# Kernel optimization log

Hardware: AMD Instinct MI355X
Metric: run time of the kernel (lower is better)

The kernel has to match this reference:

```python
import jax, jax.numpy as jnp
import numpy as np

HEAD_DIM = 32
KERNEL = 3
DILATION = 2
SCALE = HEAD_DIM ** -0.5


def _unfold(x, kernel, dilation):
    # x: [B, C, H, W] -> patches [B, C, kernel*kernel, H, W]
    # matches nn.Unfold(kernel, dilation, padding=dilation*(kernel-1)//2, stride=1)
    B, C, H, W = x.shape
    pad = dilation * (kernel - 1) // 2
    xp = jnp.pad(x, ((0, 0), (0, 0), (pad, pad), (pad, pad)))
    patches = jnp.stack(
        [xp[:, :, i * dilation:i * dilation + H, j * dilation:j * dilation + W]
         for i in range(kernel) for j in range(kernel)],
        axis=2,
    )
    return patches  # [B, C, k*k, H, W]


def setup_inputs() -> dict:
    key = jax.random.key(0)
    kq, kk, kv = jax.random.split(key, 3)
    shape = (8, 192, 56, 56)
    return {
        "q": jax.random.normal(kq, shape, dtype=jnp.float32),
        "k": jax.random.normal(kk, shape, dtype=jnp.float32),
        "v": jax.random.normal(kv, shape, dtype=jnp.float32),
    }


def reference(q, k, v):
    B, d, H, W = q.shape
    h = d // HEAD_DIM
    kk2 = KERNEL * KERNEL
    HW = H * W

    # q: [B, h, hd, HW]
    qh = q.reshape(B, h, HEAD_DIM, HW)
    # unfolded k/v: [B, h, hd, k*k, HW]
    kp = _unfold(k, KERNEL, DILATION).reshape(B, h, HEAD_DIM, kk2, HW)
    vp = _unfold(v, KERNEL, DILATION).reshape(B, h, HEAD_DIM, kk2, HW)

    attn = jnp.einsum('bhdn,bhdkn->bhnk', qh, kp) * SCALE
    attn = jax.nn.softmax(attn, axis=-1)
    # dropout p=0 (eval): no-op

    # [B, h, HW, hd]
    out = jnp.einsum('bhnk,bhdkn->bhnd', attn, vp)
    # transpose(1,2).reshape(B,H,W,d): channel order = head-major
    out = out.transpose(0, 2, 1, 3).reshape(B, H, W, d)
    return out
```

## Files before the change

kernel.cpp:

```cpp
#include <hip/hip_runtime.h>

#define NH 6
#define HEAD_DIM 32
#define CCH 192
#define HH 56
#define WW 56
#define HWSZ (HH * WW)
#define KPOS 9
#define SCALE 0.17677669529663687f
#define XPAD 61
#define ROWSZ (HEAD_DIM * XPAD)

__global__ __launch_bounds__(256, 3) void dilate_attn_lds(
    const float* __restrict__ q,
    const float* __restrict__ k,
    const float* __restrict__ v,
    float* __restrict__ out)
{
    __shared__ float ks[3 * ROWSZ];
    __shared__ float vs[3 * ROWSZ];

    const int bh = blockIdx.x % 48;
    const int y  = blockIdx.x / 48;
    const int t  = threadIdx.x;

    const int px = t >> 2;
    const int c  = t & 3;
    const bool active = px < WW;

    float qreg[8];
    if (active) {
        const float* qb = q + ((size_t)bh * HEAD_DIM + 8 * c) * HWSZ + y * WW + px;
#pragma unroll
        for (int j = 0; j < 8; j++) qreg[j] = qb[j * HWSZ];
    }

    const size_t plane = (size_t)bh * HEAD_DIM * HWSZ;
#pragma unroll
    for (int r = 0; r < 3; r++) {
        const int sy = y + 2 * r - 2;
        float* kd = ks + r * ROWSZ;
        float* vd = vs + r * ROWSZ;
        if (sy >= 0 && sy < HH) {
            const float* kg = k + plane + sy * WW;
            const float* vg = v + plane + sy * WW;
#pragma unroll
            for (int i = 0; i < 7; i++) {
                const int idx = t + 256 * i;
                const int d = idx / WW;
                const int x = idx - d * WW;
                const float kvv = kg[d * HWSZ + x];
                const float vvv = vg[d * HWSZ + x];
                kd[d * XPAD + x + 2] = kvv;
                vd[d * XPAD + x + 2] = vvv;
            }
            if (t < 128) {
                const int d  = t >> 2;
                const int xc = t & 3;
                const int xp = (xc < 2) ? xc : (56 + xc);
                kd[d * XPAD + xp] = 0.0f;
                vd[d * XPAD + xp] = 0.0f;
            }
        } else {
#pragma unroll
            for (int i = 0; i < 8; i++) {
                const int idx = t + 256 * i;
                if (idx < ROWSZ) { kd[idx] = 0.0f; vd[idx] = 0.0f; }
            }
        }
    }
    __syncthreads();

    if (!active) return;

    float lg[KPOS];
#pragma unroll
    for (int r = 0; r < 3; r++) {
        const float* kr = ks + r * ROWSZ + (8 * c) * XPAD + px;
        float a0 = 0.f, a1 = 0.f, a2 = 0.f;
#pragma unroll
        for (int j = 0; j < 8; j++) {
            const float* p = kr + j * XPAD;
            const float qj = qreg[j];
            a0 = fmaf(qj, p[0], a0);
            a1 = fmaf(qj, p[2], a1);
            a2 = fmaf(qj, p[4], a2);
        }
        lg[3 * r + 0] = a0;
        lg[3 * r + 1] = a1;
        lg[3 * r + 2] = a2;
    }

#pragma unroll
    for (int kk = 0; kk < KPOS; kk++) {
        float s = lg[kk];
        s += __shfl_xor(s, 1);
        s += __shfl_xor(s, 2);
        lg[kk] = s * SCALE;
    }

    float m = lg[0];
#pragma unroll
    for (int kk = 1; kk < KPOS; kk++) m = fmaxf(m, lg[kk]);
    float ssum = 0.f;
    float w[KPOS];
#pragma unroll
    for (int kk = 0; kk < KPOS; kk++) {
        w[kk] = __expf(lg[kk] - m);
        ssum += w[kk];
    }
    const float inv = 1.f / ssum;
#pragma unroll
    for (int kk = 0; kk < KPOS; kk++) w[kk] *= inv;

    float acc[8];
#pragma unroll
    for (int j = 0; j < 8; j++) acc[j] = 0.f;
#pragma unroll
    for (int r = 0; r < 3; r++) {
        const float* vr = vs + r * ROWSZ + (8 * c) * XPAD + px;
        const float w0 = w[3 * r + 0];
        const float w1 = w[3 * r + 1];
        const float w2 = w[3 * r + 2];
#pragma unroll
        for (int j = 0; j < 8; j++) {
            const float* p = vr + j * XPAD;
            float a = acc[j];
            a = fmaf(w0, p[0], a);
            a = fmaf(w1, p[2], a);
            a = fmaf(w2, p[4], a);
            acc[j] = a;
        }
    }

    const int h = bh % NH;
    const int b = bh / NH;
    float* ob = out + ((size_t)((b * HH + y) * WW + px)) * CCH
                    + h * HEAD_DIM + 8 * c;
    reinterpret_cast<float4*>(ob)[0] = make_float4(acc[0], acc[1], acc[2], acc[3]);
    reinterpret_cast<float4*>(ob)[1] = make_float4(acc[4], acc[5], acc[6], acc[7]);
}

extern "C" void kernel_launch(void* const* d_in, const int* in_sizes, int n_in,
                              void* d_out, int out_size, void* d_ws, size_t ws_size,
                              hipStream_t stream) {
    const float* q = (const float*)d_in[0];
    const float* k = (const float*)d_in[1];
    const float* v = (const float*)d_in[2];
    float* out = (float*)d_out;

    const int blocks = 48 * HH;
    dilate_attn_lds<<<blocks, 256, 0, stream>>>(q, k, v, out);
}
```

Measured before the change: 108.2 us.

## Process two same-parity output rows per block to share staged K/V rows

Each block now handles two output rows y0 and y0+2 with 512 threads, staging four dilated K/V source rows in LDS instead of three per single row. This cuts redundant global loads of K/V (two of the three rows are shared) and halves the block count. It raises LDS use per block to about 62KB, which may limit occupancy, and out-of-range rows are zero-filled via predicated loads.

```diff
diff --git a/kernel.cpp b/kernel.cpp
--- a/kernel.cpp
+++ b/kernel.cpp
@@ -10,85 +10,84 @@
 #define SCALE 0.17677669529663687f
 #define XPAD 61
 #define ROWSZ (HEAD_DIM * XPAD)
+#define NROWS 4
+#define PAIRS 14
 
-__global__ __launch_bounds__(256, 3) void dilate_attn_lds(
+__global__ __launch_bounds__(512, 4) void dilate_attn_pair(
     const float* __restrict__ q,
     const float* __restrict__ k,
     const float* __restrict__ v,
     float* __restrict__ out)
 {
-    __shared__ float ks[3 * ROWSZ];
-    __shared__ float vs[3 * ROWSZ];
+    __shared__ float ks[NROWS * ROWSZ];
+    __shared__ float vs[NROWS * ROWSZ];
 
-    const int bh = blockIdx.x % 48;
-    const int y  = blockIdx.x / 48;
-    const int t  = threadIdx.x;
+    const int bh       = blockIdx.x % 48;
+    const int pair_lin = blockIdx.x / 48;
+    const int parity   = pair_lin / PAIRS;
+    const int p        = pair_lin % PAIRS;
+    const int y0       = 4 * p + parity;
+    const int t        = threadIdx.x;
 
-    const int px = t >> 2;
-    const int c  = t & 3;
-    const bool active = px < WW;
+    const size_t plane = (size_t)bh * HEAD_DIM * HWSZ;
+#pragma unroll
+    for (int i = 0; i < 14; i++) {
+        const int e   = t + 512 * i;
+        const int r   = e / 1792;
+        const int rem = e - r * 1792;
+        const int d   = rem / WW;
+        const int x   = rem - d * WW;
+        const int sy  = y0 - 2 + 2 * r;
+        const bool okr = (sy >= 0) & (sy < HH);
+        const size_t g = plane + (size_t)d * HWSZ + (okr ? sy : 0) * WW + x;
+        const float kvv = okr ? k[g] : 0.0f;
+        const float vvv = okr ? v[g] : 0.0f;
+        const int a = r * ROWSZ + d * XPAD + x + 2;
+        ks[a] = kvv;
+        vs[a] = vvv;
+    }
+    {
+        const int r  = t >> 7;
+        const int rs = t & 127;
+        const int d  = rs >> 2;
+        const int xc = rs & 3;
+        const int xp = (xc < 2) ? xc : (56 + xc);
+        ks[r * ROWSZ + d * XPAD + xp] = 0.0f;
+        vs[r * ROWSZ + d * XPAD + xp] = 0.0f;
+    }
+    __syncthreads();
+
+    const int w2 = t >> 8;
+    const int tt = t & 255;
+    const int px = tt >> 2;
+    const int c  = tt & 3;
+    if (px >= WW) return;
+
+    const int y = y0 + 2 * w2;
 
     float qreg[8];
-    if (active) {
-        const float* qb = q + ((size_t)bh * HEAD_DIM + 8 * c) * HWSZ + y * WW + px;
+    {
+        const float* qb = q + plane + (size_t)(8 * c) * HWSZ + y * WW + px;
 #pragma unroll
         for (int j = 0; j < 8; j++) qreg[j] = qb[j * HWSZ];
     }
 
-    const size_t plane = (size_t)bh * HEAD_DIM * HWSZ;
-#pragma unroll
-    for (int r = 0; r < 3; r++) {
-        const int sy = y + 2 * r - 2;
-        float* kd = ks + r * ROWSZ;
-        float* vd = vs + r * ROWSZ;
-        if (sy >= 0 && sy < HH) {
-            const float* kg = k + plane + sy * WW;
-            const float* vg = v + plane + sy * WW;
-#pragma unroll
-            for (int i = 0; i < 7; i++) {
-                const int idx = t + 256 * i;
-                const int d = idx / WW;
-                const int x = idx - d * WW;
-                const float kvv = kg[d * HWSZ + x];
-                const float vvv = vg[d * HWSZ + x];
-                kd[d * XPAD + x + 2] = kvv;
-                vd[d * XPAD + x + 2] = vvv;
-            }
-            if (t < 128) {
-                const int d  = t >> 2;
-                const int xc = t & 3;
-                const int xp = (xc < 2) ? xc : (56 + xc);
-                kd[d * XPAD + xp] = 0.0f;
-                vd[d * XPAD + xp] = 0.0f;
-            }
-        } else {
-#pragma unroll
-            for (int i = 0; i < 8; i++) {
-                const int idx = t + 256 * i;
-                if (idx < ROWSZ) { kd[idx] = 0.0f; vd[idx] = 0.0f; }
-            }
-        }
-    }
-    __syncthreads();
-
-    if (!active) return;
-
     float lg[KPOS];
 #pragma unroll
-    for (int r = 0; r < 3; r++) {
-        const float* kr = ks + r * ROWSZ + (8 * c) * XPAD + px;
+    for (int rr = 0; rr < 3; rr++) {
+        const float* kr = ks + (w2 + rr) * ROWSZ + (8 * c) * XPAD + px;
         float a0 = 0.f, a1 = 0.f, a2 = 0.f;
 #pragma unroll
         for (int j = 0; j < 8; j++) {
-            const float* p = kr + j * XPAD;
+            const float* pp = kr + j * XPAD;
             const float qj = qreg[j];
-            a0 = fmaf(qj, p[0], a0);
-            a1 = fmaf(qj, p[2], a1);
-            a2 = fmaf(qj, p[4], a2);
+            a0 = fmaf(qj, pp[0], a0);
+            a1 = fmaf(qj, pp[2], a1);
+            a2 = fmaf(qj, pp[4], a2);
         }
-        lg[3 * r + 0] = a0;
-        lg[3 * r + 1] = a1;
-        lg[3 * r + 2] = a2;
+        lg[3 * rr + 0] = a0;
+        lg[3 * rr + 1] = a1;
+        lg[3 * rr + 2] = a2;
     }
 
 #pragma unroll
@@ -117,18 +116,18 @@
 #pragma unroll
     for (int j = 0; j < 8; j++) acc[j] = 0.f;
 #pragma unroll
-    for (int r = 0; r < 3; r++) {
-        const float* vr = vs + r * ROWSZ + (8 * c) * XPAD + px;
-        const float w0 = w[3 * r + 0];
-        const float w1 = w[3 * r + 1];
-        const float w2 = w[3 * r + 2];
+    for (int rr = 0; rr < 3; rr++) {
+        const float* vr = vs + (w2 + rr) * ROWSZ + (8 * c) * XPAD + px;
+        const float w0 = w[3 * rr + 0];
+        const float w1 = w[3 * rr + 1];
+        const float w2f = w[3 * rr + 2];
 #pragma unroll
         for (int j = 0; j < 8; j++) {
-            const float* p = vr + j * XPAD;
+            const float* pp = vr + j * XPAD;
             float a = acc[j];
-            a = fmaf(w0, p[0], a);
-            a = fmaf(w1, p[2], a);
-            a = fmaf(w2, p[4], a);
+            a = fmaf(w0,  pp[0], a);
+            a = fmaf(w1,  pp[2], a);
+            a = fmaf(w2f, pp[4], a);
             acc[j] = a;
         }
     }
@@ -149,6 +148,6 @@
     const float* v = (const float*)d_in[2];
     float* out = (float*)d_out;
 
-    const int blocks = 48 * HH;
-    dilate_attn_lds<<<blocks, 256, 0, stream>>>(q, k, v, out);
+    const int blocks = 48 * 2 * PAIRS;
+    dilate_attn_pair<<<blocks, 512, 0, stream>>>(q, k, v, out);
 }
```

New measurement: 116.5 us. 7.7% more time.

## Process four same-parity rows per block with rolling LDS K/V ring buffer

Applied to the files above, without the earlier changes.

Each block now handles four output rows of the same parity (stride 2), keeping a three-slot ring of K/V rows in LDS. Only one new K/V row is loaded per output row instead of three, and the next row's loads are prefetched into registers while the current row computes. This cuts redundant global reads of K and V by about a factor of three. In exchange the grid shrinks to 672 blocks, each with extra barriers and more register pressure under a tighter launch bound.

```diff
diff --git a/kernel.cpp b/kernel.cpp
--- a/kernel.cpp
+++ b/kernel.cpp
@@ -10,135 +10,175 @@
 #define SCALE 0.17677669529663687f
 #define XPAD 61
 #define ROWSZ (HEAD_DIM * XPAD)
+#define JROWS 4
+#define STRIPS 7
 
-__global__ __launch_bounds__(256, 3) void dilate_attn_lds(
+__global__ __launch_bounds__(256, 4) void dilate_attn_roll(
     const float* __restrict__ q,
     const float* __restrict__ k,
     const float* __restrict__ v,
     float* __restrict__ out)
 {
-    __shared__ float ks[3 * ROWSZ];
-    __shared__ float vs[3 * ROWSZ];
+    __shared__ float ks[3][ROWSZ];
+    __shared__ float vs[3][ROWSZ];
 
-    const int bh = blockIdx.x % 48;
-    const int y  = blockIdx.x / 48;
-    const int t  = threadIdx.x;
+    const int bh     = blockIdx.x % 48;
+    const int ps     = blockIdx.x / 48;
+    const int parity = ps / STRIPS;
+    const int s      = ps % STRIPS;
+    const int y0     = parity + 8 * s;
+    const int t      = threadIdx.x;
 
+    const size_t plane = (size_t)bh * HEAD_DIM * HWSZ;
     const int px = t >> 2;
     const int c  = t & 3;
     const bool active = px < WW;
 
-    float qreg[8];
-    if (active) {
-        const float* qb = q + ((size_t)bh * HEAD_DIM + 8 * c) * HWSZ + y * WW + px;
+    int sd[7], sx[7];
 #pragma unroll
-        for (int j = 0; j < 8; j++) qreg[j] = qb[j * HWSZ];
+    for (int i = 0; i < 7; i++) {
+        const int e = t + 256 * i;
+        sd[i] = e / WW;
+        sx[i] = e - sd[i] * WW;
     }
 
-    const size_t plane = (size_t)bh * HEAD_DIM * HWSZ;
+    float qcur[8];
+    if (active) {
+        const float* qb = q + plane + (size_t)(8 * c) * HWSZ + (size_t)y0 * WW + px;
+#pragma unroll
+        for (int j = 0; j < 8; j++) qcur[j] = qb[j * HWSZ];
+    }
+
+    for (int e = t; e < 3 * HEAD_DIM * 4; e += 256) {
+        const int slot = e >> 7;
+        const int rr   = e & 127;
+        const int d    = rr >> 2;
+        const int xc   = rr & 3;
+        const int xp   = (xc < 2) ? xc : (56 + xc);
+        ks[slot][d * XPAD + xp] = 0.0f;
+        vs[slot][d * XPAD + xp] = 0.0f;
+    }
+
+    float kpre[7], vpre[7];
 #pragma unroll
     for (int r = 0; r < 3; r++) {
-        const int sy = y + 2 * r - 2;
-        float* kd = ks + r * ROWSZ;
-        float* vd = vs + r * ROWSZ;
-        if (sy >= 0 && sy < HH) {
-            const float* kg = k + plane + sy * WW;
-            const float* vg = v + plane + sy * WW;
+        const int ky   = y0 - 2 + 2 * r;
+        const bool okr = (ky >= 0) && (ky < HH);
 #pragma unroll
-            for (int i = 0; i < 7; i++) {
-                const int idx = t + 256 * i;
-                const int d = idx / WW;
-                const int x = idx - d * WW;
-                const float kvv = kg[d * HWSZ + x];
-                const float vvv = vg[d * HWSZ + x];
-                kd[d * XPAD + x + 2] = kvv;
-                vd[d * XPAD + x + 2] = vvv;
-            }
-            if (t < 128) {
-                const int d  = t >> 2;
-                const int xc = t & 3;
-                const int xp = (xc < 2) ? xc : (56 + xc);
-                kd[d * XPAD + xp] = 0.0f;
-                vd[d * XPAD + xp] = 0.0f;
-            }
-        } else {
+        for (int i = 0; i < 7; i++) {
+            const size_t g = plane + (size_t)sd[i] * HWSZ + (size_t)(okr ? ky : 0) * WW + sx[i];
+            kpre[i] = okr ? k[g] : 0.0f;
+            vpre[i] = okr ? v[g] : 0.0f;
+        }
 #pragma unroll
-            for (int i = 0; i < 8; i++) {
-                const int idx = t + 256 * i;
-                if (idx < ROWSZ) { kd[idx] = 0.0f; vd[idx] = 0.0f; }
-            }
+        for (int i = 0; i < 7; i++) {
+            const int a = sd[i] * XPAD + sx[i] + 2;
+            ks[r][a] = kpre[i];
+            vs[r][a] = vpre[i];
         }
     }
     __syncthreads();
 
-    if (!active) return;
+    float qnxt[8];
+#pragma unroll
+    for (int j = 0; j < JROWS; j++) {
+        const int y = y0 + 2 * j;
 
-    float lg[KPOS];
+        if (j < 3) {
+            const int ky   = y0 + 4 + 2 * j;
+            const bool okr = (ky < HH);
 #pragma unroll
-    for (int r = 0; r < 3; r++) {
-        const float* kr = ks + r * ROWSZ + (8 * c) * XPAD + px;
-        float a0 = 0.f, a1 = 0.f, a2 = 0.f;
+            for (int i = 0; i < 7; i++) {
+                const size_t g = plane + (size_t)sd[i] * HWSZ + (size_t)(okr ? ky : 0) * WW + sx[i];
+                kpre[i] = okr ? k[g] : 0.0f;
+                vpre[i] = okr ? v[g] : 0.0f;
+            }
+            if (active) {
+                const float* qb = q + plane + (size_t)(8 * c) * HWSZ + (size_t)(y + 2) * WW + px;
 #pragma unroll
-        for (int j = 0; j < 8; j++) {
-            const float* p = kr + j * XPAD;
-            const float qj = qreg[j];
-            a0 = fmaf(qj, p[0], a0);
-            a1 = fmaf(qj, p[2], a1);
-            a2 = fmaf(qj, p[4], a2);
+                for (int jj = 0; jj < 8; jj++) qnxt[jj] = qb[jj * HWSZ];
+            }
         }
-        lg[3 * r + 0] = a0;
-        lg[3 * r + 1] = a1;
-        lg[3 * r + 2] = a2;
+
+        if (active) {
+            float lg[KPOS];
+#pragma unroll
+            for (int rp = 0; rp < 3; rp++) {
+                const float* kr = &ks[(j + rp) % 3][(8 * c) * XPAD + px];
+                float a0 = 0.f, a1 = 0.f, a2 = 0.f;
+#pragma unroll
+                for (int j8 = 0; j8 < 8; j8++) {
+                    const float* p  = kr + j8 * XPAD;
+                    const float qj = qcur[j8];
+                    a0 = fmaf(qj, p[0], a0);
+                    a1 = fmaf(qj, p[2], a1);
+                    a2 = fmaf(qj, p[4], a2);
+                }
+                lg[3 * rp + 0] = a0;
+                lg[3 * rp + 1] = a1;
+                lg[3 * rp + 2] = a2;
+            }
+#pragma unroll
+            for (int kk = 0; kk < KPOS; kk++) {
+                float sm = lg[kk];
+                sm += __shfl_xor(sm, 1);
+                sm += __shfl_xor(sm, 2);
+                lg[kk] = sm * SCALE;
+            }
+            float m = lg[0];
+#pragma unroll
+            for (int kk = 1; kk < KPOS; kk++) m = fmaxf(m, lg[kk]);
+            float ssum = 0.f;
+#pragma unroll
+            for (int kk = 0; kk < KPOS; kk++) {
+                lg[kk] = __expf(lg[kk] - m);
+                ssum += lg[kk];
+            }
+            const float inv = 1.f / ssum;
+
+            float acc[8];
+#pragma unroll
+            for (int jj = 0; jj < 8; jj++) acc[jj] = 0.f;
+#pragma unroll
+            for (int rp = 0; rp < 3; rp++) {
+                const float* vr = &vs[(j + rp) % 3][(8 * c) * XPAD + px];
+                const float w0 = lg[3 * rp + 0] * inv;
+                const float w1 = lg[3 * rp + 1] * inv;
+                const float w2 = lg[3 * rp + 2] * inv;
+#pragma unroll
+                for (int jj = 0; jj < 8; jj++) {
+                    const float* p = vr + jj * XPAD;
+                    float a = acc[jj];
+                    a = fmaf(w0, p[0], a);
+                    a = fmaf(w1, p[2], a);
+                    a = fmaf(w2, p[4], a);
+                    acc[jj] = a;
+                }
+            }
+
+            const int h = bh % NH;
+            const int b = bh / NH;
+            float* ob = out + ((size_t)((b * HH + y) * WW + px)) * CCH
+                            + h * HEAD_DIM + 8 * c;
+            reinterpret_cast<float4*>(ob)[0] = make_float4(acc[0], acc[1], acc[2], acc[3]);
+            reinterpret_cast<float4*>(ob)[1] = make_float4(acc[4], acc[5], acc[6], acc[7]);
+        }
+
+        __syncthreads();
+
+        if (j < 3) {
+#pragma unroll
+            for (int i = 0; i < 7; i++) {
+                const int a = sd[i] * XPAD + sx[i] + 2;
+                ks[j % 3][a] = kpre[i];
+                vs[j % 3][a] = vpre[i];
+            }
+#pragma unroll
+            for (int jj = 0; jj < 8; jj++) qcur[jj] = qnxt[jj];
+        }
+
+        __syncthreads();
     }
-
-#pragma unroll
-    for (int kk = 0; kk < KPOS; kk++) {
-        float s = lg[kk];
-        s += __shfl_xor(s, 1);
-        s += __shfl_xor(s, 2);
-        lg[kk] = s * SCALE;
-    }
-
-    float m = lg[0];
-#pragma unroll
-    for (int kk = 1; kk < KPOS; kk++) m = fmaxf(m, lg[kk]);
-    float ssum = 0.f;
-    float w[KPOS];
-#pragma unroll
-    for (int kk = 0; kk < KPOS; kk++) {
-        w[kk] = __expf(lg[kk] - m);
-        ssum += w[kk];
-    }
-    const float inv = 1.f / ssum;
-#pragma unroll
-    for (int kk = 0; kk < KPOS; kk++) w[kk] *= inv;
-
-    float acc[8];
-#pragma unroll
-    for (int j = 0; j < 8; j++) acc[j] = 0.f;
-#pragma unroll
-    for (int r = 0; r < 3; r++) {
-        const float* vr = vs + r * ROWSZ + (8 * c) * XPAD + px;
-        const float w0 = w[3 * r + 0];
-        const float w1 = w[3 * r + 1];
-        const float w2 = w[3 * r + 2];
-#pragma unroll
-        for (int j = 0; j < 8; j++) {
-            const float* p = vr + j * XPAD;
-            float a = acc[j];
-            a = fmaf(w0, p[0], a);
-            a = fmaf(w1, p[2], a);
-            a = fmaf(w2, p[4], a);
-            acc[j] = a;
-        }
-    }
-
-    const int h = bh % NH;
-    const int b = bh / NH;
-    float* ob = out + ((size_t)((b * HH + y) * WW + px)) * CCH
-                    + h * HEAD_DIM + 8 * c;
-    reinterpret_cast<float4*>(ob)[0] = make_float4(acc[0], acc[1], acc[2], acc[3]);
-    reinterpret_cast<float4*>(ob)[1] = make_float4(acc[4], acc[5], acc[6], acc[7]);
 }
 
 extern "C" void kernel_launch(void* const* d_in, const int* in_sizes, int n_in,
@@ -149,6 +189,6 @@
     const float* v = (const float*)d_in[2];
     float* out = (float*)d_out;
 
-    const int blocks = 48 * HH;
-    dilate_attn_lds<<<blocks, 256, 0, stream>>>(q, k, v, out);
+    const int blocks = 48 * 2 * STRIPS;
+    dilate_attn_roll<<<blocks, 256, 0, stream>>>(q, k, v, out);
 }
```

Measured after the change: 105.7 us. 2.3% less time.

## Compute two same-parity output rows per block sharing one LDS buffer for K then V

Applied to the files above, without the earlier changes.

Each block now handles two output rows of the same parity (y0 and y0+2), so the four K/V source rows they need are loaded once and shared. The loads of K/V per output row fall from three rows to two. K rows are staged first, V is prefetched into registers while the logits are computed, and V then overwrites the same LDS buffer. This halves shared memory per block so occupancy can rise, at the cost of many more live registers and an extra barrier.

```diff
diff --git a/kernel.cpp b/kernel.cpp
--- a/kernel.cpp
+++ b/kernel.cpp
@@ -10,135 +10,172 @@
 #define SCALE 0.17677669529663687f
 #define XPAD 61
 #define ROWSZ (HEAD_DIM * XPAD)
+#define NR 4
+#define STRIPS 14
 
-__global__ __launch_bounds__(256, 3) void dilate_attn_lds(
+__global__ __launch_bounds__(256, 5) void dilate_attn_v9(
     const float* __restrict__ q,
     const float* __restrict__ k,
     const float* __restrict__ v,
     float* __restrict__ out)
 {
-    __shared__ float ks[3 * ROWSZ];
-    __shared__ float vs[3 * ROWSZ];
+    __shared__ float buf[NR * ROWSZ];
 
-    const int bh = blockIdx.x % 48;
-    const int y  = blockIdx.x / 48;
-    const int t  = threadIdx.x;
+    const int bh     = blockIdx.x % 48;
+    const int r1     = blockIdx.x / 48;
+    const int parity = r1 / STRIPS;
+    const int si     = r1 % STRIPS;
+    const int y0     = parity + 4 * si;
+    const int t      = threadIdx.x;
 
+    const size_t plane = (size_t)bh * HEAD_DIM * HWSZ;
     const int px = t >> 2;
     const int c  = t & 3;
     const bool active = px < WW;
 
-    float qreg[8];
-    if (active) {
-        const float* qb = q + ((size_t)bh * HEAD_DIM + 8 * c) * HWSZ + y * WW + px;
+    int goff[7], aoff[7];
 #pragma unroll
-        for (int j = 0; j < 8; j++) qreg[j] = qb[j * HWSZ];
+    for (int i = 0; i < 7; i++) {
+        const int e = t + 256 * i;
+        const int d = e / WW;
+        const int x = e - d * WW;
+        goff[i] = d * HWSZ + x;
+        aoff[i] = d * XPAD + x + 2;
     }
 
-    const size_t plane = (size_t)bh * HEAD_DIM * HWSZ;
+    int   roff[NR];
+    bool  rok[NR];
 #pragma unroll
-    for (int r = 0; r < 3; r++) {
-        const int sy = y + 2 * r - 2;
-        float* kd = ks + r * ROWSZ;
-        float* vd = vs + r * ROWSZ;
-        if (sy >= 0 && sy < HH) {
-            const float* kg = k + plane + sy * WW;
-            const float* vg = v + plane + sy * WW;
+    for (int r = 0; r < NR; r++) {
+        const int ky = y0 - 2 + 2 * r;
+        rok[r]  = (ky >= 0) && (ky < HH);
+        roff[r] = (rok[r] ? ky : 0) * WW;
+    }
+
+    float qa[8], qb[8];
+    if (active) {
+        const float* q0 = q + plane + (size_t)(8 * c) * HWSZ + (size_t)y0 * WW + px;
+        const float* q1 = q0 + 2 * WW;
 #pragma unroll
-            for (int i = 0; i < 7; i++) {
-                const int idx = t + 256 * i;
-                const int d = idx / WW;
-                const int x = idx - d * WW;
-                const float kvv = kg[d * HWSZ + x];
-                const float vvv = vg[d * HWSZ + x];
-                kd[d * XPAD + x + 2] = kvv;
-                vd[d * XPAD + x + 2] = vvv;
+        for (int j = 0; j < 8; j++) { qa[j] = q0[j * HWSZ]; qb[j] = q1[j * HWSZ]; }
+    }
+
+    {
+        float kpre[NR][7];
+#pragma unroll
+        for (int r = 0; r < NR; r++)
+#pragma unroll
+            for (int i = 0; i < 7; i++)
+                kpre[r][i] = rok[r] ? k[plane + roff[r] + goff[i]] : 0.0f;
+#pragma unroll
+        for (int r = 0; r < NR; r++)
+#pragma unroll
+            for (int i = 0; i < 7; i++)
+                buf[r * ROWSZ + aoff[i]] = kpre[r][i];
+    }
+#pragma unroll
+    for (int ii = 0; ii < 2; ii++) {
+        const int e  = t + 256 * ii;
+        const int r  = e >> 7;
+        const int rr = e & 127;
+        const int d  = rr >> 2;
+        const int xc = rr & 3;
+        const int xp = (xc < 2) ? xc : (56 + xc);
+        buf[r * ROWSZ + d * XPAD + xp] = 0.0f;
+    }
+    __syncthreads();
+
+    float vpre[NR][7];
+#pragma unroll
+    for (int r = 0; r < NR; r++)
+#pragma unroll
+        for (int i = 0; i < 7; i++)
+            vpre[r][i] = rok[r] ? v[plane + roff[r] + goff[i]] : 0.0f;
+
+    float w0[KPOS], w1[KPOS];
+    if (active) {
+#pragma unroll
+        for (int w2 = 0; w2 < 2; w2++) {
+            float* lg = w2 ? w1 : w0;
+            const float* qr = w2 ? qb : qa;
+#pragma unroll
+            for (int rp = 0; rp < 3; rp++) {
+                const float* kr = buf + (w2 + rp) * ROWSZ + (8 * c) * XPAD + px;
+                float a0 = 0.f, a1 = 0.f, a2 = 0.f;
+#pragma unroll
+                for (int j = 0; j < 8; j++) {
+                    const float* p = kr + j * XPAD;
+                    const float qj = qr[j];
+                    a0 = fmaf(qj, p[0], a0);
+                    a1 = fmaf(qj, p[2], a1);
+                    a2 = fmaf(qj, p[4], a2);
+                }
+                lg[3 * rp + 0] = a0;
+                lg[3 * rp + 1] = a1;
+                lg[3 * rp + 2] = a2;
             }
-            if (t < 128) {
-                const int d  = t >> 2;
-                const int xc = t & 3;
-                const int xp = (xc < 2) ? xc : (56 + xc);
-                kd[d * XPAD + xp] = 0.0f;
-                vd[d * XPAD + xp] = 0.0f;
+#pragma unroll
+            for (int kk = 0; kk < KPOS; kk++) {
+                float s = lg[kk];
+                s += __shfl_xor(s, 1);
+                s += __shfl_xor(s, 2);
+                lg[kk] = s * SCALE;
             }
-        } else {
+            float m = lg[0];
 #pragma unroll
-            for (int i = 0; i < 8; i++) {
-                const int idx = t + 256 * i;
-                if (idx < ROWSZ) { kd[idx] = 0.0f; vd[idx] = 0.0f; }
+            for (int kk = 1; kk < KPOS; kk++) m = fmaxf(m, lg[kk]);
+            float ssum = 0.f;
+#pragma unroll
+            for (int kk = 0; kk < KPOS; kk++) {
+                lg[kk] = __expf(lg[kk] - m);
+                ssum += lg[kk];
             }
+            const float inv = 1.f / ssum;
+#pragma unroll
+            for (int kk = 0; kk < KPOS; kk++) lg[kk] *= inv;
         }
     }
     __syncthreads();
 
-    if (!active) return;
+#pragma unroll
+    for (int r = 0; r < NR; r++)
+#pragma unroll
+        for (int i = 0; i < 7; i++)
+            buf[r * ROWSZ + aoff[i]] = vpre[r][i];
+    __syncthreads();
 
-    float lg[KPOS];
+    if (active) {
+        const int h = bh % NH;
+        const int b = bh / NH;
 #pragma unroll
-    for (int r = 0; r < 3; r++) {
-        const float* kr = ks + r * ROWSZ + (8 * c) * XPAD + px;
-        float a0 = 0.f, a1 = 0.f, a2 = 0.f;
+        for (int w2 = 0; w2 < 2; w2++) {
+            const float* w = w2 ? w1 : w0;
+            float acc[8];
 #pragma unroll
-        for (int j = 0; j < 8; j++) {
-            const float* p = kr + j * XPAD;
-            const float qj = qreg[j];
-            a0 = fmaf(qj, p[0], a0);
-            a1 = fmaf(qj, p[2], a1);
-            a2 = fmaf(qj, p[4], a2);
-        }
-        lg[3 * r + 0] = a0;
-        lg[3 * r + 1] = a1;
-        lg[3 * r + 2] = a2;
-    }
-
+            for (int j = 0; j < 8; j++) acc[j] = 0.f;
 #pragma unroll
-    for (int kk = 0; kk < KPOS; kk++) {
-        float s = lg[kk];
-        s += __shfl_xor(s, 1);
-        s += __shfl_xor(s, 2);
-        lg[kk] = s * SCALE;
-    }
-
-    float m = lg[0];
+            for (int rp = 0; rp < 3; rp++) {
+                const float* vr = buf + (w2 + rp) * ROWSZ + (8 * c) * XPAD + px;
+                const float wa = w[3 * rp + 0];
+                const float wb = w[3 * rp + 1];
+                const float wc = w[3 * rp + 2];
 #pragma unroll
-    for (int kk = 1; kk < KPOS; kk++) m = fmaxf(m, lg[kk]);
-    float ssum = 0.f;
-    float w[KPOS];
-#pragma unroll
-    for (int kk = 0; kk < KPOS; kk++) {
-        w[kk] = __expf(lg[kk] - m);
-        ssum += w[kk];
-    }
-    const float inv = 1.f / ssum;
-#pragma unroll
-    for (int kk = 0; kk < KPOS; kk++) w[kk] *= inv;
-
-    float acc[8];
-#pragma unroll
-    for (int j = 0; j < 8; j++) acc[j] = 0.f;
-#pragma unroll
-    for (int r = 0; r < 3; r++) {
-        const float* vr = vs + r * ROWSZ + (8 * c) * XPAD + px;
-        const float w0 = w[3 * r + 0];
-        const float w1 = w[3 * r + 1];
-        const float w2 = w[3 * r + 2];
-#pragma unroll
-        for (int j = 0; j < 8; j++) {
-            const float* p = vr + j * XPAD;
-            float a = acc[j];
-            a = fmaf(w0, p[0], a);
-            a = fmaf(w1, p[2], a);
-            a = fmaf(w2, p[4], a);
-            acc[j] = a;
+                for (int j = 0; j < 8; j++) {
+                    const float* p = vr + j * XPAD;
+                    float a = acc[j];
+                    a = fmaf(wa, p[0], a);
+                    a = fmaf(wb, p[2], a);
+                    a = fmaf(wc, p[4], a);
+                    acc[j] = a;
+                }
+            }
+            const int y = y0 + 2 * w2;
+            float* ob = out + ((size_t)((b * HH + y) * WW + px)) * CCH
+                            + h * HEAD_DIM + 8 * c;
+            reinterpret_cast<float4*>(ob)[0] = make_float4(acc[0], acc[1], acc[2], acc[3]);
+            reinterpret_cast<float4*>(ob)[1] = make_float4(acc[4], acc[5], acc[6], acc[7]);
         }
     }
-
-    const int h = bh % NH;
-    const int b = bh / NH;
-    float* ob = out + ((size_t)((b * HH + y) * WW + px)) * CCH
-                    + h * HEAD_DIM + 8 * c;
-    reinterpret_cast<float4*>(ob)[0] = make_float4(acc[0], acc[1], acc[2], acc[3]);
-    reinterpret_cast<float4*>(ob)[1] = make_float4(acc[4], acc[5], acc[6], acc[7]);
 }
 
 extern "C" void kernel_launch(void* const* d_in, const int* in_sizes, int n_in,
@@ -149,6 +186,6 @@
     const float* v = (const float*)d_in[2];
     float* out = (float*)d_out;
 
-    const int blocks = 48 * HH;
-    dilate_attn_lds<<<blocks, 256, 0, stream>>>(q, k, v, out);
+    const int blocks = 48 * 2 * STRIPS;
+    dilate_attn_v9<<<blocks, 256, 0, stream>>>(q, k, v, out);
 }
```

Measured after the change: 129.9 us. +20.0%, slower.
